# Optimization experiments

Hardware: AMD Instinct MI355X
Metric: run time of the kernel (lower is better)

## Reference

```python
import jax, jax.numpy as jnp
import numpy as np

D_MODEL = 1024
NHEAD = 16
HEAD_DIM = D_MODEL // NHEAD
LN_EPS = 1e-5


def setup_inputs() -> dict:
    key = jax.random.key(0)
    ks = jax.random.split(key, 6)
    B, S = 4, 4096
    x = jax.random.normal(ks[0], (B, S, D_MODEL), dtype=jnp.float32)
    scale = 0.02
    Wq = jax.random.normal(ks[1], (D_MODEL, D_MODEL), dtype=jnp.float32) * scale
    Wv = jax.random.normal(ks[2], (D_MODEL, D_MODEL), dtype=jnp.float32) * scale
    Wo = jax.random.normal(ks[3], (D_MODEL, D_MODEL), dtype=jnp.float32) * scale
    Wg = jax.random.normal(ks[4], (D_MODEL, D_MODEL), dtype=jnp.float32) * scale
    beta = jnp.full((NHEAD,), -0.2, dtype=jnp.float32)
    ln_gamma = jnp.ones((D_MODEL,), dtype=jnp.float32)
    ln_beta = jnp.zeros((D_MODEL,), dtype=jnp.float32)
    return {"x": x, "Wq": Wq, "Wv": Wv, "Wo": Wo, "Wg": Wg,
            "beta": beta, "ln_gamma": ln_gamma, "ln_beta": ln_beta}


def _ema_scan(lam, v):
    # v: [B, S, H, D]; lam: [1, 1, H, 1]
    # s_t = lam * s_{t-1} + v_t, computed with a parallel associative scan
    # on pairs (a, b) representing the affine map s -> a*s + b.
    a = jnp.broadcast_to(lam, v.shape)

    def combine(e1, e2):
        a1, b1 = e1
        a2, b2 = e2
        return a1 * a2, a2 * b1 + b2

    _, state = jax.lax.associative_scan(combine, (a, v), axis=1)
    return state


def reference(x, Wq, Wv, Wo, Wg, beta, ln_gamma, ln_beta):
    B, S, _ = x.shape
    q = (x @ Wq.T).reshape(B, S, NHEAD, HEAD_DIM)
    v = (x @ Wv.T).reshape(B, S, NHEAD, HEAD_DIM)
    lam = jax.nn.sigmoid(beta).reshape(1, 1, NHEAD, 1).astype(v.dtype)
    state = _ema_scan(lam, v)                      # [B, S, H, D]
    y = (q * state).reshape(B, S, D_MODEL)
    # LayerNorm over last dim
    mu = jnp.mean(y, axis=-1, keepdims=True)
    var = jnp.mean(jnp.square(y - mu), axis=-1, keepdims=True)
    y = (y - mu) * jax.lax.rsqrt(var + LN_EPS) * ln_gamma + ln_beta
    gate = jax.nn.silu(x @ Wg.T)
    y = y * gate
    return y @ Wo.T
```

## Files before the change

### kernel.cpp

```cpp
#include <hip/hip_runtime.h>

#define D_MODEL 1024
#define NHEAD 16
#define LN_EPS 1e-5f
#define CHUNK 32
#define S_LEN 4096
#define NCH (S_LEN / CHUNK)

typedef unsigned short u16;
typedef __attribute__((ext_vector_type(8))) short short8;
typedef __attribute__((ext_vector_type(4))) float f32x4;

__device__ __forceinline__ u16 f2b(float f) {
  unsigned u = __builtin_bit_cast(unsigned, f);
  u += 0x7FFFu + ((u >> 16) & 1u);
  return (u16)(u >> 16);
}
__device__ __forceinline__ float b2f(u16 s) {
  return __builtin_bit_cast(float, ((unsigned)s) << 16);
}

__device__ __forceinline__ ushort4 cvt4(float4 f) {
  ushort4 o; o.x = f2b(f.x); o.y = f2b(f.y); o.z = f2b(f.z); o.w = f2b(f.w);
  return o;
}
__global__ __launch_bounds__(256) void cvt_all(
    const float4* __restrict__ x,  const float4* __restrict__ wq,
    const float4* __restrict__ wv, const float4* __restrict__ wg,
    const float4* __restrict__ wo, ushort4* __restrict__ xb,
    ushort4* __restrict__ wqvg, ushort4* __restrict__ wob,
    const float* __restrict__ beta, float* __restrict__ lam,
    int nx4, int nw4) {
  int i = blockIdx.x * blockDim.x + threadIdx.x;
  int stride = gridDim.x * blockDim.x;
  if (blockIdx.x == 0 && threadIdx.x < NHEAD) {
    float l = 1.f / (1.f + __expf(-beta[threadIdx.x]));
    lam[threadIdx.x] = l;
    lam[NHEAD + threadIdx.x] = __log2f(l);
  }
  for (int j = i; j < nx4; j += stride) xb[j] = cvt4(x[j]);
  for (int j = i; j < nw4; j += stride) wqvg[j] = cvt4(wq[j]);
  for (int j = i; j < nw4; j += stride) wqvg[nw4 + j] = cvt4(wv[j]);
  for (int j = i; j < nw4; j += stride) wqvg[2 * nw4 + j] = cvt4(wg[j]);
  for (int j = i; j < nw4; j += stride) wob[j] = cvt4(wo[j]);
}


__device__ __forceinline__ void glds16(const u16* g, const u16* l) {
  __builtin_amdgcn_global_load_lds(
      (const __attribute__((address_space(1))) unsigned*)g,
      (__attribute__((address_space(3))) unsigned*)l, 16, 0, 0);
}

#define BAR() asm volatile("s_barrier" ::: "memory")
#define SB0() __builtin_amdgcn_sched_barrier(0)

template <typename OutT, bool CARRY>
__global__ __launch_bounds__(512, 2) void gemm256(const u16* __restrict__ X,
                                                  const u16* __restrict__ W,
                                                  OutT* __restrict__ Out,
                                                  float* __restrict__ carry,
                                                  const float* __restrict__ lamlog,
                                                  int M, int N, int K) {
  __shared__ u16 sm[8][8192];
  const int tid = threadIdx.x;
  const int lane = tid & 63;
  const int wave = tid >> 6;
  const int ln15 = lane & 15, lh = lane >> 4;
  const int wr = wave >> 2, wc = wave & 3;
  const int bm = blockIdx.x * 256, bn = blockIdx.y * 256;
  const int NT = K >> 6;

  const int srow = tid >> 3;
  const int scol = ((tid & 7) ^ (srow & 7)) << 3;
  const u16* Asrc = X + (size_t)(bm + srow) * K + scol;
  const u16* Bsrc = W + (size_t)(bn + srow) * K + scol;
  const int ldsw = wave * 512;

#define STAGE(u, h, tile, src)                                          \
  { const u16* _g = (src) + (size_t)((h) * 128) * K + (tile) * 64;      \
    glds16(_g,                  &sm[u][ldsw]);                          \
    glds16(_g + (size_t)64 * K, &sm[u][ldsw + 4096]); }

  const char* smb = (const char*)&sm[0][0];
  const char* Ard = smb + wr * 16384 + ln15 * 128;
  const char* Brd = smb + (2 + (wc >> 1)) * 16384 + ((wc & 1) * 64 + ln15) * 128;
  const int swz0 = ((lh ^ (ln15 & 7)) << 4);
  const int swz1 = (((4 + lh) ^ (ln15 & 7)) << 4);

#define RD_A(DB, MM, S) (*(const short8*)(Ard + (DB) + (MM) * 2048 + (S)))
#define RD_B(DB, NN, S) (*(const short8*)(Brd + (DB) + (NN) * 2048 + (S)))

  f32x4 acc[8][4];
  f32x4 zero = {0.f, 0.f, 0.f, 0.f};
  #pragma unroll
  for (int m = 0; m < 8; ++m)
    #pragma unroll
    for (int n = 0; n < 4; ++n) acc[m][n] = zero;

  short8 a[8][2], b[4][2];

#define MFMA_Q(M0, N0)                                                        \
  SB0();                                                                      \
  __builtin_amdgcn_s_setprio(1);                                              \
  _Pragma("unroll")                                                           \
  for (int m = (M0); m < (M0) + 4; ++m)                                       \
    _Pragma("unroll")                                                         \
    for (int n = (N0); n < (N0) + 2; ++n) {                                   \
      acc[m][n] = __builtin_amdgcn_mfma_f32_16x16x32_bf16(a[m][0], b[n][0], acc[m][n], 0, 0, 0); \
      acc[m][n] = __builtin_amdgcn_mfma_f32_16x16x32_bf16(a[m][1], b[n][1], acc[m][n], 0, 0, 0); \
    }                                                                         \
  __builtin_amdgcn_s_setprio(0);                                              \
  SB0();

  STAGE(0, 0, 0, Asrc); STAGE(1, 1, 0, Asrc);
  STAGE(2, 0, 0, Bsrc); STAGE(3, 1, 0, Bsrc);
  STAGE(4, 0, 1, Asrc); STAGE(5, 1, 1, Asrc);
  asm volatile("s_waitcnt vmcnt(4)" ::: "memory");
  BAR();
  #pragma unroll
  for (int m = 0; m < 4; ++m) { a[m][0] = RD_A(0, m, swz0); a[m][1] = RD_A(0, m, swz1); }
  #pragma unroll
  for (int n = 0; n < 4; ++n) { b[n][0] = RD_B(0, n, swz0); b[n][1] = RD_B(0, n, swz1); }

  for (int t = 0; t < NT; ++t) {
    const int d = t & 1;
    const int db = d * 65536;
    const int odb = (d ^ 1) * 65536;
    const int od = (d ^ 1) * 4;
    const int sd = d * 4;
    const int tB = (t + 1 < NT) ? t + 1 : NT - 1;
    const int tA = (t + 2 < NT) ? t + 2 : NT - 1;

    a[4][0] = RD_A(db, 4, swz0); a[4][1] = RD_A(db, 4, swz1);
    a[5][0] = RD_A(db, 5, swz0); a[5][1] = RD_A(db, 5, swz1);
    STAGE(od + 2, 0, tB, Bsrc);
    MFMA_Q(0, 0)

    a[6][0] = RD_A(db, 6, swz0); a[6][1] = RD_A(db, 6, swz1);
    a[7][0] = RD_A(db, 7, swz0); a[7][1] = RD_A(db, 7, swz1);
    STAGE(od + 3, 1, tB, Bsrc);
    MFMA_Q(0, 2)
    asm volatile("s_waitcnt vmcnt(4)" ::: "memory");
    BAR();

    #pragma unroll
    for (int m = 0; m < 4; ++m) { a[m][0] = RD_A(odb, m, swz0); a[m][1] = RD_A(odb, m, swz1); }
    MFMA_Q(4, 2)
    STAGE(sd + 0, 0, tA, Asrc);
    asm volatile("s_waitcnt vmcnt(2)" ::: "memory");
    BAR();

    b[2][0] = RD_B(odb, 2, swz0); b[2][1] = RD_B(odb, 2, swz1);
    b[3][0] = RD_B(odb, 3, swz0); b[3][1] = RD_B(odb, 3, swz1);
    MFMA_Q(4, 0)
    b[0][0] = RD_B(odb, 0, swz0); b[0][1] = RD_B(odb, 0, swz1);
    b[1][0] = RD_B(odb, 1, swz0); b[1][1] = RD_B(odb, 1, swz1);
    STAGE(sd + 1, 1, tA, Asrc);
  }
#undef STAGE
#undef RD_A
#undef RD_B
#undef MFMA_Q

  #pragma unroll
  for (int m = 0; m < 8; ++m)
    #pragma unroll
    for (int n = 0; n < 4; ++n)
      #pragma unroll
      for (int r = 0; r < 4; ++r) {
        int row = bm + wr * 128 + m * 16 + lh * 4 + r;
        int col = bn + wc * 64 + n * 16 + ln15;
        float vv = acc[m][n][r];
        if constexpr (sizeof(OutT) == 2) Out[(size_t)row * N + col] = f2b(vv);
        else                             Out[(size_t)row * N + col] = vv;
      }

  if constexpr (CARRY) {
    if (bn >= 1024 && bn < 2048) {
      const int bidx = bm >> 12;
      const int chunkbase = ((bm & 4095) >> 5) + wr * 4;
      const int colbase = (bn - 1024) + wc * 64;
      const float l2h = lamlog[colbase >> 6];
      float wgt[2][4];
      #pragma unroll
      for (int mo = 0; mo < 2; ++mo)
        #pragma unroll
        for (int r = 0; r < 4; ++r)
          wgt[mo][r] = exp2f(l2h * (float)(31 - (mo * 16 + lh * 4 + r)));
      #pragma unroll
      for (int mq = 0; mq < 4; ++mq) {
        #pragma unroll
        for (int n = 0; n < 4; ++n) {
          float part = 0.f;
          #pragma unroll
          for (int mo = 0; mo < 2; ++mo)
            #pragma unroll
            for (int r = 0; r < 4; ++r)
              part += wgt[mo][r] * acc[mq * 2 + mo][n][r];
          part += __shfl_down(part, 16);
          part += __shfl_down(part, 32);
          if (lh == 0)
            carry[(size_t)(bidx * NCH + chunkbase + mq) * D_MODEL +
                  colbase + n * 16 + ln15] = part;
        }
      }
    }
  }
}

__global__ void scan_carry(float* __restrict__ carry, const float* __restrict__ lam,
                           int B, int nch) {
  int idx = blockIdx.x * blockDim.x + threadIdx.x;
  if (idx >= B * D_MODEL) return;
  int b = idx >> 10, col = idx & (D_MODEL - 1);
  float lC = exp2f(lam[NHEAD + (col >> 6)] * (float)CHUNK);
  float c = 0.f;
  #pragma unroll 4
  for (int j = 0; j < nch; ++j) {
    size_t a = ((size_t)(b * nch + j)) * D_MODEL + col;
    c = lC * c + carry[a];
    carry[a] = c;
  }
}

__global__ __launch_bounds__(256) void scan_ln(const u16* __restrict__ qvg,
    const float* __restrict__ carry, const float* __restrict__ lam,
    const float* __restrict__ gamma, const float* __restrict__ lbeta,
    u16* __restrict__ yout, int S, int nch, int ld) {
  const int bj = blockIdx.x;
  const int b = bj / nch, j = bj - b * nch;
  const int tid = threadIdx.x;
  const int col0 = tid * 4;
  const float l = lam[col0 >> 6];
  const float4 gm = *(const float4*)(gamma + col0);
  const float4 bt = *(const float4*)(lbeta + col0);

  float cp0 = 0.f, cp1 = 0.f, cp2 = 0.f, cp3 = 0.f;
  if (j > 0) {
    const float4 c4 = *(const float4*)(carry + (size_t)(bj - 1) * D_MODEL + col0);
    cp0 = c4.x; cp1 = c4.y; cp2 = c4.z; cp3 = c4.w;
  }
  float p = l;
  float s0 = 0.f, s1 = 0.f, s2 = 0.f, s3 = 0.f;
  const size_t row0 = (size_t)b * S + (size_t)j * CHUNK;
  const size_t rb0 = row0 * ld;

  ushort4 qu = *(const ushort4*)(qvg + rb0 + col0);
  ushort4 su = *(const ushort4*)(qvg + rb0 + D_MODEL + col0);
  ushort4 gu = *(const ushort4*)(qvg + rb0 + 2 * D_MODEL + col0);

  __shared__ float red[2][8];
  const int ln = tid & 63, wv = tid >> 6;

  for (int t = 0; t < CHUNK; ++t) {
    ushort4 qn, sn, gn;
    if (t + 1 < CHUNK) {
      size_t nb = rb0 + (size_t)(t + 1) * ld;
      qn = *(const ushort4*)(qvg + nb + col0);
      sn = *(const ushort4*)(qvg + nb + D_MODEL + col0);
      gn = *(const ushort4*)(qvg + nb + 2 * D_MODEL + col0);
    }
    s0 = l * s0 + b2f(su.x);
    s1 = l * s1 + b2f(su.y);
    s2 = l * s2 + b2f(su.z);
    s3 = l * s3 + b2f(su.w);
    float st0 = s0 + p * cp0, st1 = s1 + p * cp1;
    float st2 = s2 + p * cp2, st3 = s3 + p * cp3;
    float y0 = b2f(qu.x) * st0, y1 = b2f(qu.y) * st1;
    float y2 = b2f(qu.z) * st2, y3 = b2f(qu.w) * st3;
    float sum = y0 + y1 + y2 + y3;
    float sumsq = y0 * y0 + y1 * y1 + y2 * y2 + y3 * y3;
    #pragma unroll
    for (int off = 32; off > 0; off >>= 1) {
      sum += __shfl_down(sum, off);
      sumsq += __shfl_down(sumsq, off);
    }
    const int par = t & 1;
    if (ln == 0) { red[par][wv] = sum; red[par][4 + wv] = sumsq; }
    __syncthreads();
    sum = red[par][0] + red[par][1] + red[par][2] + red[par][3];
    sumsq = red[par][4] + red[par][5] + red[par][6] + red[par][7];
    float mu = sum * (1.f / 1024.f);
    float var = sumsq * (1.f / 1024.f) - mu * mu;
    float rstd = rsqrtf(var + LN_EPS);

    float g0 = b2f(gu.x), g1 = b2f(gu.y), g2 = b2f(gu.z), g3 = b2f(gu.w);
    float o0 = ((y0 - mu) * rstd * gm.x + bt.x) * (g0 / (1.f + __expf(-g0)));
    float o1 = ((y1 - mu) * rstd * gm.y + bt.y) * (g1 / (1.f + __expf(-g1)));
    float o2 = ((y2 - mu) * rstd * gm.z + bt.z) * (g2 / (1.f + __expf(-g2)));
    float o3 = ((y3 - mu) * rstd * gm.w + bt.w) * (g3 / (1.f + __expf(-g3)));
    ushort4 o; o.x = f2b(o0); o.y = f2b(o1); o.z = f2b(o2); o.w = f2b(o3);
    *(ushort4*)(yout + (row0 + t) * D_MODEL + col0) = o;

    if (t + 1 < CHUNK) { qu = qn; su = sn; gu = gn; }
    p *= l;
  }
}

extern "C" void kernel_launch(void* const* d_in, const int* in_sizes, int n_in,
                              void* d_out, int out_size, void* d_ws, size_t ws_size,
                              hipStream_t stream) {
  const float* x     = (const float*)d_in[0];
  const float* Wq    = (const float*)d_in[1];
  const float* Wv    = (const float*)d_in[2];
  const float* Wo    = (const float*)d_in[3];
  const float* Wg    = (const float*)d_in[4];
  const float* beta  = (const float*)d_in[5];
  const float* gamma = (const float*)d_in[6];
  const float* lbeta = (const float*)d_in[7];
  float* out = (float*)d_out;

  const int BS = in_sizes[0] / D_MODEL;
  const int S = S_LEN;
  const int B = BS / S;
  const int nch = NCH;
  const size_t nx = (size_t)BS * D_MODEL;
  const size_t nw = (size_t)D_MODEL * D_MODEL;
  const int N3 = 3 * D_MODEL;

  char* w = (char*)d_ws;
  u16* xb   = (u16*)w;  w += nx * 2;
  u16* wqvg = (u16*)w;  w += 3 * nw * 2;
  u16* wob  = (u16*)w;  w += nw * 2;
  u16* qvg  = (u16*)w;  w += (size_t)BS * N3 * 2;
  u16* yb   = (u16*)w;  w += nx * 2;
  float* carry = (float*)w;  w += (size_t)B * nch * D_MODEL * 4;
  float* lam = (float*)w;

  cvt_all<<<2048, 256, 0, stream>>>((const float4*)x, (const float4*)Wq,
      (const float4*)Wv, (const float4*)Wg, (const float4*)Wo,
      (ushort4*)xb, (ushort4*)wqvg, (ushort4*)wob, beta, lam,
      (int)(nx / 4), (int)(nw / 4));

  dim3 g1(BS / 256, N3 / 256);
  gemm256<u16, true><<<g1, 512, 0, stream>>>(xb, wqvg, qvg, carry, lam + NHEAD,
                                             BS, N3, D_MODEL);

  scan_carry<<<(B * D_MODEL + 255) / 256, 256, 0, stream>>>(carry, lam, B, nch);
  scan_ln<<<B * nch, 256, 0, stream>>>(qvg, carry, lam, gamma, lbeta, yb, S, nch, N3);

  dim3 g2(BS / 256, D_MODEL / 256);
  gemm256<float, false><<<g2, 512, 0, stream>>>(yb, wob, out, nullptr, nullptr,
                                                BS, D_MODEL, D_MODEL);
}
```

Before: 224.7 us.

## Fuse conversion loops, swizzle GEMM block order, widen scan_ln to 8 columns

The five fp32-to-bf16 conversion loops become one grid-stride loop over all tensors. The GEMM block index is remapped so that consecutive blocks are spread in groups of eight, which is meant to improve L2 locality across chiplets or caches. scan_ln now handles 8 columns per thread with 128 threads, using 16-byte loads and stores and a two-wave reduction, to cut per-row synchronisation and instruction overhead. The block remap assumes the grid size is divisible by eight, and fewer threads per block may reduce the latency hiding available in scan_ln.

```diff
diff --git a/kernel.cpp b/kernel.cpp
--- a/kernel.cpp
+++ b/kernel.cpp
@@ -9,6 +9,7 @@
 
 typedef unsigned short u16;
 typedef __attribute__((ext_vector_type(8))) short short8;
+typedef __attribute__((ext_vector_type(8))) unsigned short u16x8;
 typedef __attribute__((ext_vector_type(4))) float f32x4;
 
 __device__ __forceinline__ u16 f2b(float f) {
@@ -38,11 +39,19 @@
     lam[threadIdx.x] = l;
     lam[NHEAD + threadIdx.x] = __log2f(l);
   }
-  for (int j = i; j < nx4; j += stride) xb[j] = cvt4(x[j]);
-  for (int j = i; j < nw4; j += stride) wqvg[j] = cvt4(wq[j]);
-  for (int j = i; j < nw4; j += stride) wqvg[nw4 + j] = cvt4(wv[j]);
-  for (int j = i; j < nw4; j += stride) wqvg[2 * nw4 + j] = cvt4(wg[j]);
-  for (int j = i; j < nw4; j += stride) wob[j] = cvt4(wo[j]);
+  const int total = nx4 + 4 * nw4;
+  for (int j = i; j < total; j += stride) {
+    float4 f; ushort4* dst;
+    if (j < nx4) { f = x[j]; dst = xb + j; }
+    else {
+      int k = j - nx4;
+      int w = k / nw4, o = k - w * nw4;
+      const float4* s = (w == 0) ? wq : (w == 1) ? wv : (w == 2) ? wg : wo;
+      f = s[o];
+      dst = (w < 3) ? (wqvg + (size_t)w * nw4 + o) : (wob + o);
+    }
+    *dst = cvt4(f);
+  }
 }
 
 
@@ -68,7 +77,12 @@
   const int wave = tid >> 6;
   const int ln15 = lane & 15, lh = lane >> 4;
   const int wr = wave >> 2, wc = wave & 3;
-  const int bm = blockIdx.x * 256, bn = blockIdx.y * 256;
+
+  const int lin = blockIdx.y * gridDim.x + blockIdx.x;
+  const int cpx = (gridDim.x * gridDim.y) >> 3;
+  const int sw = (lin & 7) * cpx + (lin >> 3);
+  const int bm = (sw % gridDim.x) * 256;
+  const int bn = (sw / gridDim.x) * 256;
   const int NT = K >> 6;
 
   const int srow = tid >> 3;
@@ -224,76 +238,79 @@
   }
 }
 
-__global__ __launch_bounds__(256) void scan_ln(const u16* __restrict__ qvg,
+__global__ __launch_bounds__(128) void scan_ln(const u16* __restrict__ qvg,
     const float* __restrict__ carry, const float* __restrict__ lam,
     const float* __restrict__ gamma, const float* __restrict__ lbeta,
     u16* __restrict__ yout, int S, int nch, int ld) {
   const int bj = blockIdx.x;
   const int b = bj / nch, j = bj - b * nch;
   const int tid = threadIdx.x;
-  const int col0 = tid * 4;
+  const int col0 = tid * 8;
   const float l = lam[col0 >> 6];
-  const float4 gm = *(const float4*)(gamma + col0);
-  const float4 bt = *(const float4*)(lbeta + col0);
-
-  float cp0 = 0.f, cp1 = 0.f, cp2 = 0.f, cp3 = 0.f;
+
+  float gm[8], bt[8];
+  #pragma unroll
+  for (int i = 0; i < 8; ++i) { gm[i] = gamma[col0 + i]; bt[i] = lbeta[col0 + i]; }
+
+  float cp[8] = {0.f, 0.f, 0.f, 0.f, 0.f, 0.f, 0.f, 0.f};
   if (j > 0) {
-    const float4 c4 = *(const float4*)(carry + (size_t)(bj - 1) * D_MODEL + col0);
-    cp0 = c4.x; cp1 = c4.y; cp2 = c4.z; cp3 = c4.w;
-  }
+    const float* cb = carry + (size_t)(bj - 1) * D_MODEL + col0;
+    #pragma unroll
+    for (int i = 0; i < 8; ++i) cp[i] = cb[i];
+  }
+  float s[8] = {0.f, 0.f, 0.f, 0.f, 0.f, 0.f, 0.f, 0.f};
   float p = l;
-  float s0 = 0.f, s1 = 0.f, s2 = 0.f, s3 = 0.f;
   const size_t row0 = (size_t)b * S + (size_t)j * CHUNK;
-  const size_t rb0 = row0 * ld;
-
-  ushort4 qu = *(const ushort4*)(qvg + rb0 + col0);
-  ushort4 su = *(const ushort4*)(qvg + rb0 + D_MODEL + col0);
-  ushort4 gu = *(const ushort4*)(qvg + rb0 + 2 * D_MODEL + col0);
-
-  __shared__ float red[2][8];
+  const u16* base = qvg + row0 * ld + col0;
+
+  u16x8 qu = *(const u16x8*)(base);
+  u16x8 vu = *(const u16x8*)(base + D_MODEL);
+  u16x8 gu = *(const u16x8*)(base + 2 * D_MODEL);
+
+  __shared__ float red[2][2][2];
   const int ln = tid & 63, wv = tid >> 6;
 
   for (int t = 0; t < CHUNK; ++t) {
-    ushort4 qn, sn, gn;
+    u16x8 qn, vn, gn;
     if (t + 1 < CHUNK) {
-      size_t nb = rb0 + (size_t)(t + 1) * ld;
-      qn = *(const ushort4*)(qvg + nb + col0);
-      sn = *(const ushort4*)(qvg + nb + D_MODEL + col0);
-      gn = *(const ushort4*)(qvg + nb + 2 * D_MODEL + col0);
-    }
-    s0 = l * s0 + b2f(su.x);
-    s1 = l * s1 + b2f(su.y);
-    s2 = l * s2 + b2f(su.z);
-    s3 = l * s3 + b2f(su.w);
-    float st0 = s0 + p * cp0, st1 = s1 + p * cp1;
-    float st2 = s2 + p * cp2, st3 = s3 + p * cp3;
-    float y0 = b2f(qu.x) * st0, y1 = b2f(qu.y) * st1;
-    float y2 = b2f(qu.z) * st2, y3 = b2f(qu.w) * st3;
-    float sum = y0 + y1 + y2 + y3;
-    float sumsq = y0 * y0 + y1 * y1 + y2 * y2 + y3 * y3;
+      const u16* nb = base + (size_t)(t + 1) * ld;
+      qn = *(const u16x8*)(nb);
+      vn = *(const u16x8*)(nb + D_MODEL);
+      gn = *(const u16x8*)(nb + 2 * D_MODEL);
+    }
+    float y[8];
+    float sum = 0.f, sumsq = 0.f;
+    #pragma unroll
+    for (int i = 0; i < 8; ++i) {
+      s[i] = l * s[i] + b2f(vu[i]);
+      float st = s[i] + p * cp[i];
+      float yy = b2f(qu[i]) * st;
+      y[i] = yy; sum += yy; sumsq += yy * yy;
+    }
     #pragma unroll
     for (int off = 32; off > 0; off >>= 1) {
       sum += __shfl_down(sum, off);
       sumsq += __shfl_down(sumsq, off);
     }
     const int par = t & 1;
-    if (ln == 0) { red[par][wv] = sum; red[par][4 + wv] = sumsq; }
+    if (ln == 0) { red[par][0][wv] = sum; red[par][1][wv] = sumsq; }
     __syncthreads();
-    sum = red[par][0] + red[par][1] + red[par][2] + red[par][3];
-    sumsq = red[par][4] + red[par][5] + red[par][6] + red[par][7];
+    sum = red[par][0][0] + red[par][0][1];
+    sumsq = red[par][1][0] + red[par][1][1];
     float mu = sum * (1.f / 1024.f);
     float var = sumsq * (1.f / 1024.f) - mu * mu;
     float rstd = rsqrtf(var + LN_EPS);
 
-    float g0 = b2f(gu.x), g1 = b2f(gu.y), g2 = b2f(gu.z), g3 = b2f(gu.w);
-    float o0 = ((y0 - mu) * rstd * gm.x + bt.x) * (g0 / (1.f + __expf(-g0)));
-    float o1 = ((y1 - mu) * rstd * gm.y + bt.y) * (g1 / (1.f + __expf(-g1)));
-    float o2 = ((y2 - mu) * rstd * gm.z + bt.z) * (g2 / (1.f + __expf(-g2)));
-    float o3 = ((y3 - mu) * rstd * gm.w + bt.w) * (g3 / (1.f + __expf(-g3)));
-    ushort4 o; o.x = f2b(o0); o.y = f2b(o1); o.z = f2b(o2); o.w = f2b(o3);
-    *(ushort4*)(yout + (row0 + t) * D_MODEL + col0) = o;
-
-    if (t + 1 < CHUNK) { qu = qn; su = sn; gu = gn; }
+    u16x8 o;
+    #pragma unroll
+    for (int i = 0; i < 8; ++i) {
+      float g = b2f(gu[i]);
+      float oo = ((y[i] - mu) * rstd * gm[i] + bt[i]) * (g / (1.f + __expf(-g)));
+      o[i] = f2b(oo);
+    }
+    *(u16x8*)(yout + (row0 + t) * D_MODEL + col0) = o;
+
+    if (t + 1 < CHUNK) { qu = qn; vu = vn; gu = gn; }
     p *= l;
   }
 }
@@ -338,7 +355,7 @@
                                              BS, N3, D_MODEL);
 
   scan_carry<<<(B * D_MODEL + 255) / 256, 256, 0, stream>>>(carry, lam, B, nch);
-  scan_ln<<<B * nch, 256, 0, stream>>>(qvg, carry, lam, gamma, lbeta, yb, S, nch, N3);
+  scan_ln<<<B * nch, 128, 0, stream>>>(qvg, carry, lam, gamma, lbeta, yb, S, nch, N3);
 
   dim3 g2(BS / 256, D_MODEL / 256);
   gemm256<float, false><<<g2, 512, 0, stream>>>(yb, wob, out, nullptr, nullptr,
```

After: 247.7 us. +10.2%, slower.
